# Optimization experiments

Hardware: AMD Instinct MI355X
Metric: run time of the kernel (lower is better)

## Reference

```python
import jax, jax.numpy as jnp
import numpy as np
from jax import lax

NPOINT = 1024
RADIUS = 0.2
NSAMPLE = 32
BN_EPS = 1e-5


def fps(xyz, npoint):
    """Deterministic farthest point sampling (start index 0). xyz: (B,N,3) -> (B,npoint) int32."""
    B, N, _ = xyz.shape

    def step(carry, _):
        distance, farthest = carry
        centroid = jnp.take_along_axis(xyz, farthest[:, None, None], axis=1)  # (B,1,3)
        d = jnp.sum((xyz - centroid) ** 2, axis=-1)  # (B,N)
        distance = jnp.minimum(distance, d)
        nxt = jnp.argmax(distance, axis=-1).astype(jnp.int32)
        return (distance, nxt), farthest

    init = (jnp.full((B, N), jnp.inf, dtype=xyz.dtype), jnp.zeros((B,), jnp.int32))
    _, idxs = lax.scan(step, init, None, length=npoint)  # (npoint, B)
    return jnp.transpose(idxs)  # (B, npoint)


def ball_query(radius, nsample, xyz, new_xyz):
    """Deterministic ball query: first nsample in-radius indices (sorted), padded with first hit.
    xyz: (B,N,3), new_xyz: (B,S,3) -> (B,S,nsample) int32."""
    B, N, _ = xyz.shape
    # squared distances via GEMM form to avoid (B,S,N,3) intermediate
    sqr = (jnp.sum(new_xyz ** 2, -1)[:, :, None]
           + jnp.sum(xyz ** 2, -1)[:, None, :]
           - 2.0 * jnp.einsum('bsd,bnd->bsn', new_xyz, xyz))  # (B,S,N)
    idx = jnp.where(sqr <= radius ** 2, jnp.arange(N, dtype=jnp.int32), N)
    idx = jnp.sort(idx, axis=-1)[:, :, :nsample]  # (B,S,K)
    first = idx[:, :, :1]
    first = jnp.where(first == N, 0, first)  # no point in radius -> index 0
    return jnp.where(idx == N, first, idx)


def setup_inputs() -> dict:
    key = jax.random.key(0)
    ks = jax.random.split(key, 8)
    B, N, Cin = 16, 4096, 64
    xyz = jax.random.uniform(ks[0], (B, N, 3), dtype=jnp.float32)
    points = jax.random.normal(ks[1], (B, Cin, N), dtype=jnp.float32)
    chans = [Cin + 3, 64, 64, 128]
    d = {"xyz": xyz, "points": points}
    for i in range(3):
        d[f"w{i}"] = jax.random.normal(ks[2 + i], (chans[i + 1], chans[i]), dtype=jnp.float32) / np.float32(np.sqrt(chans[i]))
        d[f"g{i}"] = jnp.ones((chans[i + 1],), dtype=jnp.float32)
        d[f"b{i}"] = jnp.zeros((chans[i + 1],), dtype=jnp.float32)
    return d


def _forward(xyz, points, params):
    B, N, _ = xyz.shape
    idx = fps(xyz, NPOINT)                                     # (B,S)
    new_xyz = jnp.take_along_axis(xyz, idx[:, :, None], axis=1)  # (B,S,3)
    gidx = ball_query(RADIUS, NSAMPLE, xyz, new_xyz)             # (B,S,K)
    gather = jax.vmap(lambda p, i: p[i])
    grouped_xyz = gather(xyz, gidx) - new_xyz[:, :, None, :]     # (B,S,K,3)
    grouped_pts = gather(jnp.transpose(points, (0, 2, 1)), gidx)  # (B,S,K,C)
    feats = jnp.concatenate([grouped_xyz, grouped_pts], axis=-1)  # (B,S,K,3+C)
    for (w, g, b) in params:
        feats = jnp.einsum('oc,bskc->bsko', w, feats)
        mean = jnp.mean(feats, axis=(0, 1, 2))
        var = jnp.var(feats, axis=(0, 1, 2))
        feats = (feats - mean) * (g * lax.rsqrt(var + BN_EPS)) + b  # BatchNorm (batch stats)
        feats = jax.nn.relu(feats)
    feats = jnp.max(feats, axis=2)               # (B,S,Cout) max-pool over neighbors
    return new_xyz, jnp.transpose(feats, (0, 2, 1))  # (B,Cout,S) channel-first like torch


def reference(xyz, points, w0, g0, b0, w1, g1, b1, w2, g2, b2):
    params = [(w0, g0, b0), (w1, g1, b1), (w2, g2, b2)]
    return _forward(xyz, points, params)
```

## Files before the change

kernel.cpp:

```cpp
#include <hip/hip_runtime.h>

#define DI static __device__ __forceinline__

typedef float v2f __attribute__((ext_vector_type(2)));
typedef __attribute__((ext_vector_type(8))) short bf16x8;
typedef __attribute__((ext_vector_type(4))) float f32x4;

DI unsigned short f2bf(float f) {
  unsigned int u = __float_as_uint(f);
  u = (u + 0x7fffu + ((u >> 16) & 1u)) >> 16;
  return (unsigned short)u;
}
DI float bf2f(unsigned short h) { return __uint_as_float(((unsigned int)h) << 16); }

#define DPP_MAXU(v, ctrl)                                                      \
  {                                                                            \
    unsigned o_ = (unsigned)__builtin_amdgcn_update_dpp((int)(v), (int)(v),    \
                                                        (ctrl), 0xf, 0xf, false); \
    (v) = (o_ > (v)) ? o_ : (v);                                               \
  }
#define DPP_MINU(v, ctrl)                                                      \
  {                                                                            \
    unsigned o_ = (unsigned)__builtin_amdgcn_update_dpp((int)(v), (int)(v),    \
                                                        (ctrl), 0xf, 0xf, false); \
    (v) = (o_ < (v)) ? o_ : (v);                                               \
  }

__global__ __launch_bounds__(256) void fps_kernel(const float* __restrict__ xyz,
                                                  float* __restrict__ newxyz) {
  const int b = blockIdx.x;
  const int t = threadIdx.x;
  const int lane = t & 63, wid = t >> 6;
  const float* X = xyz + (size_t)b * 4096 * 3;
  __shared__ float XL[4096 * 3];
  __shared__ int FI[1024];
  __shared__ unsigned long long slot[2][4];
  for (int idx = t; idx < 12288; idx += 256) XL[idx] = X[idx];
  v2f px[8], py[8], pz[8], dist[8];
#pragma unroll
  for (int q = 0; q < 8; ++q) {
    int i0 = t + (q << 9);
    int i1 = i0 + 256;
    px[q] = (v2f){X[i0 * 3 + 0], X[i1 * 3 + 0]};
    py[q] = (v2f){X[i0 * 3 + 1], X[i1 * 3 + 1]};
    pz[q] = (v2f){X[i0 * 3 + 2], X[i1 * 3 + 2]};
    dist[q] = (v2f){3.402823466e38f, 3.402823466e38f};
  }
  __syncthreads();
  float cx = XL[0], cy = XL[1], cz = XL[2];
  int fi = 0;
  for (int s = 0; s < 1024; ++s) {
    if (t == 0) FI[s] = fi;
    float bv = -1.0f;
    unsigned int bi = 0;
    v2f cxv = (v2f){cx, cx}, cyv = (v2f){cy, cy}, czv = (v2f){cz, cz};
#pragma unroll
    for (int q = 0; q < 8; ++q) {
#pragma clang fp contract(off)
      v2f dx = px[q] - cxv;
      v2f dy = py[q] - cyv;
      v2f dz = pz[q] - czv;
      v2f d = (dx * dx + dy * dy) + dz * dz;
#if __has_builtin(__builtin_elementwise_min)
      v2f nd = __builtin_elementwise_min(dist[q], d);
#else
      v2f nd;
      nd.x = fminf(dist[q].x, d.x);
      nd.y = fminf(dist[q].y, d.y);
#endif
      dist[q] = nd;
      float n0 = nd.x, n1 = nd.y;
      bool c0 = (n0 > bv);
      bv = c0 ? n0 : bv;
      bi = c0 ? (unsigned)(t + (q << 9)) : bi;
      bool c1 = (n1 > bv);
      bv = c1 ? n1 : bv;
      bi = c1 ? (unsigned)(t + (q << 9) + 256) : bi;
    }
    unsigned vb = __float_as_uint(bv);
    unsigned m = vb;
    DPP_MAXU(m, 0x111);
    DPP_MAXU(m, 0x112);
    DPP_MAXU(m, 0x114);
    DPP_MAXU(m, 0x118);
    DPP_MAXU(m, 0x142);
    DPP_MAXU(m, 0x143);
    unsigned wmax = (unsigned)__builtin_amdgcn_readlane((int)m, 63);
    unsigned ik = (vb == wmax) ? bi : 0xFFFFFFFFu;
    DPP_MINU(ik, 0x111);
    DPP_MINU(ik, 0x112);
    DPP_MINU(ik, 0x114);
    DPP_MINU(ik, 0x118);
    DPP_MINU(ik, 0x142);
    DPP_MINU(ik, 0x143);
    unsigned widx = (unsigned)__builtin_amdgcn_readlane((int)ik, 63);
    const int p = s & 1;
    if (lane == 0)
      slot[p][wid] = ((unsigned long long)wmax << 32) | (unsigned long long)(~widx);
    __syncthreads();
    unsigned long long k0 = slot[p][0], k1 = slot[p][1];
    unsigned long long k2 = slot[p][2], k3 = slot[p][3];
    unsigned long long m01 = (k0 >= k1) ? k0 : k1;
    unsigned long long m23 = (k2 >= k3) ? k2 : k3;
    unsigned long long win = (m01 >= m23) ? m01 : m23;
    fi = (int)(~(unsigned int)win);
    cx = XL[fi * 3 + 0];
    cy = XL[fi * 3 + 1];
    cz = XL[fi * 3 + 2];
  }
  __syncthreads();
  float* out = newxyz + (size_t)b * 1024 * 3;
  for (int s2 = t; s2 < 1024; s2 += 256) {
    int f = FI[s2];
    out[s2 * 3 + 0] = XL[f * 3 + 0];
    out[s2 * 3 + 1] = XL[f * 3 + 1];
    out[s2 * 3 + 2] = XL[f * 3 + 2];
  }
}

__global__ __launch_bounds__(256) void p0_kernel(const float* __restrict__ points,
                                                 const float* __restrict__ w0,
                                                 float* __restrict__ P0) {
  const int b = blockIdx.x >> 6;
  const int n0 = (blockIdx.x & 63) << 6;
  const int t = threadIdx.x;
  __shared__ float W[64][64];
  for (int idx = t; idx < 4096; idx += 256) {
    int c = idx >> 6, o = idx & 63;
    W[c][o] = w0[o * 67 + 3 + c];
  }
  __syncthreads();
  const int i = t >> 4, j = t & 15;
  const float* Pb = points + (size_t)b * 64 * 4096 + n0 + 4 * i;
  float acc[4][4] = {};
  for (int c = 0; c < 64; ++c) {
    float4 xv = *(const float4*)(Pb + (size_t)c * 4096);
    float4 wv = *(const float4*)&W[c][4 * j];
    float xr[4] = {xv.x, xv.y, xv.z, xv.w};
    float wr[4] = {wv.x, wv.y, wv.z, wv.w};
#pragma unroll
    for (int rr = 0; rr < 4; ++rr)
#pragma unroll
      for (int oi = 0; oi < 4; ++oi) acc[rr][oi] = fmaf(xr[rr], wr[oi], acc[rr][oi]);
  }
#pragma unroll
  for (int rr = 0; rr < 4; ++rr) {
    float4 vv = make_float4(acc[rr][0], acc[rr][1], acc[rr][2], acc[rr][3]);
    *(float4*)(P0 + ((size_t)b * 4096 + n0 + 4 * i + rr) * 64 + 4 * j) = vv;
  }
}

__global__ __launch_bounds__(256) void ballquery_stats0_kernel(
    const float* __restrict__ xyz, const float* __restrict__ newxyz,
    const float* __restrict__ P0, const float* __restrict__ w0,
    int* __restrict__ gidx, float* __restrict__ partials0) {
  const int t = threadIdx.x;
  const int lane = t & 63, w = t >> 6;
  const int gid = blockIdx.x * 4 + w;
  const int b = gid >> 10;
  __shared__ int sel[4][32];
  __shared__ float red[4][128];
  const float* Xb = xyz + (size_t)b * 4096 * 3;
  const float cx = newxyz[(size_t)gid * 3 + 0];
  const float cy = newxyz[(size_t)gid * 3 + 1];
  const float cz = newxyz[(size_t)gid * 3 + 2];
  const float cs = __fadd_rn(__fadd_rn(__fmul_rn(cx, cx), __fmul_rn(cy, cy)), __fmul_rn(cz, cz));
  int cnt = 0, first = 0;
  bool found = false;
  for (int base = 0; base < 4096; base += 64) {
    int i = base + lane;
    float x = Xb[i * 3 + 0], y = Xb[i * 3 + 1], z = Xb[i * 3 + 2];
    float xs = __fadd_rn(__fadd_rn(__fmul_rn(x, x), __fmul_rn(y, y)), __fmul_rn(z, z));
    float dot = fmaf(cz, z, fmaf(cy, y, __fmul_rn(cx, x)));
    float sqr = __fsub_rn(__fadd_rn(cs, xs), __fmul_rn(2.0f, dot));
    bool ok = sqr <= 0.04f;
    unsigned long long mask = __ballot(ok);
    if (!found && mask != 0ull) { first = base + __builtin_ctzll(mask); found = true; }
    int pre = __popcll(mask & ((1ull << lane) - 1ull));
    int pos = cnt + pre;
    if (ok && pos < 32) sel[w][pos] = i;
    cnt += (int)__popcll(mask);
    if (cnt >= 32) break;
  }
  if (cnt < 32) {
    int pad = found ? first : 0;
    for (int p = cnt + lane; p < 32; p += 64) sel[w][p] = pad;
  }
  __syncthreads();
  if (lane < 32) gidx[(size_t)gid * 32 + lane] = sel[w][lane];
  const int c = lane;
  float wx = w0[c * 67 + 0], wy = w0[c * 67 + 1], wz = w0[c * 67 + 2];
  float ssum = 0.f, ssq = 0.f;
  const float* P0b = P0 + (size_t)b * 4096 * 64;
  for (int k = 0; k < 32; ++k) {
    int g = sel[w][k];
    float gx = Xb[g * 3 + 0] - cx, gy = Xb[g * 3 + 1] - cy, gz = Xb[g * 3 + 2] - cz;
    float a0 = fmaf(wx, gx, fmaf(wy, gy, fmaf(wz, gz, P0b[(size_t)g * 64 + c])));
    ssum += a0;
    ssq = fmaf(a0, a0, ssq);
  }
  red[w][c] = ssum;
  red[w][c + 64] = ssq;
  __syncthreads();
  if (t < 128) {
    float acc = red[0][t] + red[1][t] + red[2][t] + red[3][t];
    partials0[(size_t)t * 4096 + blockIdx.x] = acc;
  }
}

__global__ __launch_bounds__(256) void finalize_kernel(
    const float* __restrict__ partials, int C, int nblk,
    const float* __restrict__ gamma, const float* __restrict__ beta,
    float* __restrict__ scale, float* __restrict__ shift) {
  const int c = blockIdx.x, t = threadIdx.x;
  double s1 = 0.0, s2 = 0.0;
  for (int k = t; k < nblk; k += 256) {
    s1 += (double)partials[(size_t)c * nblk + k];
    s2 += (double)partials[(size_t)(C + c) * nblk + k];
  }
  __shared__ double r1[256], r2[256];
  r1[t] = s1;
  r2[t] = s2;
  __syncthreads();
  for (int off = 128; off > 0; off >>= 1) {
    if (t < off) { r1[t] += r1[t + off]; r2[t] += r2[t + off]; }
    __syncthreads();
  }
  if (t == 0) {
    const double M = 524288.0;
    double mean = r1[0] / M;
    double var = r2[0] / M - mean * mean;
    if (var < 0.0) var = 0.0;
    float sc = gamma[c] * (float)(1.0 / sqrt(var + 1e-5));
    scale[c] = sc;
    shift[c] = beta[c] - (float)mean * sc;
  }
}

__global__ __launch_bounds__(256) void p2_kernel(
    const float* __restrict__ xyz, const float* __restrict__ newxyz,
    const float* __restrict__ P0, const int* __restrict__ gidx,
    const float* __restrict__ w0, const float* __restrict__ w1,
    const float* __restrict__ sc0g, const float* __restrict__ sh0g,
    unsigned short* __restrict__ act1, float* __restrict__ partials1) {
  __shared__ float W1s[64][64];
  __shared__ float Xs[64][64];
  __shared__ float w0x[64], w0y[64], w0z[64], sc0[64], sh0[64];
  __shared__ float Sred[256][8];
  const int t = threadIdx.x;
  for (int idx = t; idx < 4096; idx += 256) {
    int c = idx >> 6, o = idx & 63;
    W1s[c][o] = w1[o * 64 + c];
  }
  if (t < 64) {
    w0x[t] = w0[t * 67 + 0];
    w0y[t] = w0[t * 67 + 1];
    w0z[t] = w0[t * 67 + 2];
    sc0[t] = sc0g[t];
    sh0[t] = sh0g[t];
  }
  __syncthreads();
  const int i = t >> 4, j = t & 15;
  const int rl = t >> 2, cq = t & 3;
  float ssum[4] = {}, ssq[4] = {};
  for (int tile = 0; tile < 8; ++tile) {
    const int rowbase = (blockIdx.x * 8 + tile) << 6;
    {
      int r = rowbase + rl;
      int b = r >> 15, s = (r >> 5) & 1023;
      int g = gidx[r];
      const float* Pt = xyz + ((size_t)b * 4096 + g) * 3;
      const float* Ct = newxyz + ((size_t)b * 1024 + s) * 3;
      float dx = Pt[0] - Ct[0], dy = Pt[1] - Ct[1], dz = Pt[2] - Ct[2];
      const float* p0r = P0 + ((size_t)b * 4096 + g) * 64 + cq * 16;
      const float4* p4 = (const float4*)p0r;
      float4 a0 = p4[0], a1 = p4[1], a2 = p4[2], a3 = p4[3];
      float pv[16] = {a0.x, a0.y, a0.z, a0.w, a1.x, a1.y, a1.z, a1.w,
                      a2.x, a2.y, a2.z, a2.w, a3.x, a3.y, a3.z, a3.w};
#pragma unroll
      for (int cc = 0; cc < 16; ++cc) {
        int c = cq * 16 + cc;
        float a = fmaf(w0x[c], dx, fmaf(w0y[c], dy, fmaf(w0z[c], dz, pv[cc])));
        Xs[c][rl] = fmaxf(0.f, fmaf(a, sc0[c], sh0[c]));
      }
    }
    __syncthreads();
    float acc[4][4] = {};
#pragma unroll 4
    for (int c = 0; c < 64; ++c) {
      float4 xv = *(const float4*)&Xs[c][4 * i];
      float4 wv = *(const float4*)&W1s[c][4 * j];
      float xr[4] = {xv.x, xv.y, xv.z, xv.w};
      float wr[4] = {wv.x, wv.y, wv.z, wv.w};
#pragma unroll
      for (int rr = 0; rr < 4; ++rr)
#pragma unroll
        for (int oi = 0; oi < 4; ++oi) acc[rr][oi] = fmaf(xr[rr], wr[oi], acc[rr][oi]);
    }
#pragma unroll
    for (int rr = 0; rr < 4; ++rr) {
      size_t r = (size_t)rowbase + 4 * i + rr;
      ushort4 pk;
      float y0 = acc[rr][0], y1 = acc[rr][1], y2 = acc[rr][2], y3 = acc[rr][3];
      ssum[0] += y0; ssq[0] = fmaf(y0, y0, ssq[0]);
      ssum[1] += y1; ssq[1] = fmaf(y1, y1, ssq[1]);
      ssum[2] += y2; ssq[2] = fmaf(y2, y2, ssq[2]);
      ssum[3] += y3; ssq[3] = fmaf(y3, y3, ssq[3]);
      pk.x = f2bf(y0); pk.y = f2bf(y1); pk.z = f2bf(y2); pk.w = f2bf(y3);
      *(ushort4*)(act1 + r * 64 + 4 * j) = pk;
    }
    __syncthreads();
  }
#pragma unroll
  for (int oi = 0; oi < 4; ++oi) { Sred[t][oi] = ssum[oi]; Sred[t][4 + oi] = ssq[oi]; }
  __syncthreads();
  if (t < 64) {
    int jj = t >> 2, oi = t & 3;
    float s1 = 0.f, s2 = 0.f;
#pragma unroll
    for (int ii = 0; ii < 16; ++ii) {
      s1 += Sred[ii * 16 + jj][oi];
      s2 += Sred[ii * 16 + jj][4 + oi];
    }
    partials1[(size_t)t * 1024 + blockIdx.x] = s1;
    partials1[(size_t)(64 + t) * 1024 + blockIdx.x] = s2;
  }
}

__global__ __launch_bounds__(256) void p3_kernel(
    const unsigned short* __restrict__ act1, const float* __restrict__ w2,
    const float* __restrict__ sc1g, const float* __restrict__ sh1g,
    float* __restrict__ partials2, float* __restrict__ gmx,
    float* __restrict__ gmn) {
  __shared__ unsigned short W2T[128 * 72];
  __shared__ unsigned short A[64 * 72];
  __shared__ float Mred[4][132], Nred[4][132];
  __shared__ float S1r[4][132], S2r[4][132];
  __shared__ float sc1[64], sh1[64];
  const int t = threadIdx.x;
  const int lane = t & 63, w = t >> 6;
  const int quad = lane >> 4, l15 = lane & 15;
  for (int idx = t; idx < 8192; idx += 256) {
    int o = idx >> 6, c = idx & 63;
    W2T[o * 72 + c] = f2bf(w2[o * 64 + c]);
  }
  if (t < 64) { sc1[t] = sc1g[t]; sh1[t] = sh1g[t]; }
  __syncthreads();
  const int rl = t >> 2, cq = t & 3;
  float ssum[8] = {}, ssq[8] = {};
  for (int tile = 0; tile < 8; ++tile) {
    const int rowbase = (blockIdx.x * 8 + tile) << 6;
    {
      size_t r = (size_t)rowbase + rl;
      const uint4* pr = (const uint4*)(act1 + r * 64 + cq * 16);
      uint4 aa = pr[0], bb = pr[1];
      unsigned int uu[8] = {aa.x, aa.y, aa.z, aa.w, bb.x, bb.y, bb.z, bb.w};
      unsigned int pk[8];
#pragma unroll
      for (int q = 0; q < 8; ++q) {
        int c = cq * 16 + 2 * q;
        float v0 = bf2f((unsigned short)(uu[q] & 0xffffu));
        float v1 = bf2f((unsigned short)(uu[q] >> 16));
        float r0 = fmaxf(0.f, fmaf(v0, sc1[c], sh1[c]));
        float r1 = fmaxf(0.f, fmaf(v1, sc1[c + 1], sh1[c + 1]));
        pk[q] = (unsigned)f2bf(r0) | ((unsigned)f2bf(r1) << 16);
      }
      uint4* dst = (uint4*)&A[rl * 72 + cq * 16];
      dst[0] = make_uint4(pk[0], pk[1], pk[2], pk[3]);
      dst[1] = make_uint4(pk[4], pk[5], pk[6], pk[7]);
    }
    __syncthreads();
    const unsigned short* Arow = &A[(w * 16 + l15) * 72 + quad * 8];
    bf16x8 a0 = *(const bf16x8*)(Arow);
    bf16x8 a1 = *(const bf16x8*)(Arow + 32);
    f32x4 acc[8];
#pragma unroll
    for (int nt = 0; nt < 8; ++nt) {
      const unsigned short* Brow = &W2T[(nt * 16 + l15) * 72 + quad * 8];
      bf16x8 b0 = *(const bf16x8*)(Brow);
      bf16x8 b1 = *(const bf16x8*)(Brow + 32);
      f32x4 c0 = {0.f, 0.f, 0.f, 0.f};
      c0 = __builtin_amdgcn_mfma_f32_16x16x32_bf16(a0, b0, c0, 0, 0, 0);
      c0 = __builtin_amdgcn_mfma_f32_16x16x32_bf16(a1, b1, c0, 0, 0, 0);
      acc[nt] = c0;
    }
#pragma unroll
    for (int nt = 0; nt < 8; ++nt) {
      float y0 = acc[nt][0], y1 = acc[nt][1], y2 = acc[nt][2], y3 = acc[nt][3];
      ssum[nt] += ((y0 + y1) + (y2 + y3));
      ssq[nt] = fmaf(y0, y0, ssq[nt]);
      ssq[nt] = fmaf(y1, y1, ssq[nt]);
      ssq[nt] = fmaf(y2, y2, ssq[nt]);
      ssq[nt] = fmaf(y3, y3, ssq[nt]);
      float mx = fmaxf(fmaxf(y0, y1), fmaxf(y2, y3));
      float mn = fminf(fminf(y0, y1), fminf(y2, y3));
      mx = fmaxf(mx, __shfl_xor(mx, 16, 64));
      mx = fmaxf(mx, __shfl_xor(mx, 32, 64));
      mn = fminf(mn, __shfl_xor(mn, 16, 64));
      mn = fminf(mn, __shfl_xor(mn, 32, 64));
      if (quad == 0) {
        Mred[w][nt * 16 + l15] = mx;
        Nred[w][nt * 16 + l15] = mn;
      }
    }
    __syncthreads();
    {
      int o = t & 127, g = t >> 7;
      float mx = fmaxf(Mred[2 * g][o], Mred[2 * g + 1][o]);
      float mn = fminf(Nred[2 * g][o], Nred[2 * g + 1][o]);
      int bb2 = rowbase >> 15;
      int ss2 = ((rowbase >> 5) & 1023) + g;
      size_t oidx = ((size_t)bb2 * 128 + o) * 1024 + ss2;
      gmx[oidx] = mx;
      gmn[oidx] = mn;
    }
    __syncthreads();
  }
#pragma unroll
  for (int nt = 0; nt < 8; ++nt) {
    float s1 = ssum[nt];
    s1 += __shfl_xor(s1, 16, 64);
    s1 += __shfl_xor(s1, 32, 64);
    float s2 = ssq[nt];
    s2 += __shfl_xor(s2, 16, 64);
    s2 += __shfl_xor(s2, 32, 64);
    if (quad == 0) {
      S1r[w][nt * 16 + l15] = s1;
      S2r[w][nt * 16 + l15] = s2;
    }
  }
  __syncthreads();
  if (t < 128) {
    int o = t;
    float s1 = S1r[0][o] + S1r[1][o] + S1r[2][o] + S1r[3][o];
    float s2 = S2r[0][o] + S2r[1][o] + S2r[2][o] + S2r[3][o];
    partials2[(size_t)o * 1024 + blockIdx.x] = s1;
    partials2[(size_t)(128 + o) * 1024 + blockIdx.x] = s2;
  }
}

__global__ __launch_bounds__(256) void p4f_kernel(
    const float* __restrict__ gmx, const float* __restrict__ gmn,
    const float* __restrict__ sc2g, const float* __restrict__ sh2g,
    float* __restrict__ feats) {
  const int bo = blockIdx.x >> 2;
  const int s = ((blockIdx.x & 3) << 8) + threadIdx.x;
  const int o = bo & 127;
  const float sc = sc2g[o], sh = sh2g[o];
  size_t idx = (size_t)bo * 1024 + s;
  float v = (sc >= 0.f) ? gmx[idx] : gmn[idx];
  feats[idx] = fmaxf(0.f, fmaf(v, sc, sh));
}

extern "C" void kernel_launch(void* const* d_in, const int* in_sizes, int n_in,
                              void* d_out, int out_size, void* d_ws, size_t ws_size,
                              hipStream_t stream) {
  const float* xyz = (const float*)d_in[0];
  const float* points = (const float*)d_in[1];
  const float* w0 = (const float*)d_in[2];
  const float* g0 = (const float*)d_in[3];
  const float* b0 = (const float*)d_in[4];
  const float* w1 = (const float*)d_in[5];
  const float* g1 = (const float*)d_in[6];
  const float* b1 = (const float*)d_in[7];
  const float* w2 = (const float*)d_in[8];
  const float* g2 = (const float*)d_in[9];
  const float* b2 = (const float*)d_in[10];

  float* out = (float*)d_out;
  float* newxyz = out;
  float* feats = out + 49152;

  char* ws = (char*)d_ws;
  float* P0 = (float*)ws;
  float* gmx = (float*)ws;
  float* gmn = (float*)(ws + (size_t)(8u << 20));
  int* gidx = (int*)(ws + (size_t)(16u << 20));
  unsigned short* act1 = (unsigned short*)(ws + (size_t)(18u << 20));
  float* partials0 = (float*)(ws + (size_t)(82u << 20));
  float* partials1 = (float*)(ws + (size_t)(84u << 20));
  float* partials2 = (float*)(ws + (size_t)(85u << 20));
  float* sc0 = (float*)(ws + (size_t)(86u << 20));
  float* sh0 = sc0 + 128;
  float* sc1 = sc0 + 256;
  float* sh1 = sc0 + 384;
  float* sc2 = sc0 + 512;
  float* sh2 = sc0 + 640;

  fps_kernel<<<16, 256, 0, stream>>>(xyz, newxyz);
  p0_kernel<<<1024, 256, 0, stream>>>(points, w0, P0);
  ballquery_stats0_kernel<<<4096, 256, 0, stream>>>(xyz, newxyz, P0, w0, gidx, partials0);
  finalize_kernel<<<64, 256, 0, stream>>>(partials0, 64, 4096, g0, b0, sc0, sh0);
  p2_kernel<<<1024, 256, 0, stream>>>(xyz, newxyz, P0, gidx, w0, w1, sc0, sh0, act1, partials1);
  finalize_kernel<<<64, 256, 0, stream>>>(partials1, 64, 1024, g1, b1, sc1, sh1);
  p3_kernel<<<1024, 256, 0, stream>>>(act1, w2, sc1, sh1, partials2, gmx, gmn);
  finalize_kernel<<<128, 256, 0, stream>>>(partials2, 128, 1024, g2, b2, sc2, sh2);
  p4f_kernel<<<8192, 256, 0, stream>>>(gmx, gmn, sc2, sh2, feats);
}
```

Before: 922.0 us.

## Use bf16 MFMA for layer-1 GEMM and packed f32 ops in FPS

The second-layer 64x64 GEMM in p2_kernel moves from scalar FP32 FMA over shared-memory tiles to bf16 MFMA 16x16x32, with inputs and weights converted to bf16 in padded LDS. The BN statistics reduction now uses wave shuffles instead of a large shared array. Separately, the FPS distance computation is forced onto v_pk_add/v_pk_mul inline asm. The MFMA path lowers precision of the layer-1 input, and the act1 stores become scattered 2-byte writes, which may reduce store efficiency.

Measured after the change: 938.8 us. About the same (+1.8%).

```diff
diff --git a/kernel.cpp b/kernel.cpp
--- a/kernel.cpp
+++ b/kernel.cpp
@@ -12,6 +12,22 @@
   return (unsigned short)u;
 }
 DI float bf2f(unsigned short h) { return __uint_as_float(((unsigned int)h) << 16); }
+
+DI v2f pk_sub(v2f a, v2f b) {
+  v2f d;
+  asm("v_pk_add_f32 %0, %1, %2 neg_lo:[0,1] neg_hi:[0,1]" : "=v"(d) : "v"(a), "v"(b));
+  return d;
+}
+DI v2f pk_mul(v2f a, v2f b) {
+  v2f d;
+  asm("v_pk_mul_f32 %0, %1, %2" : "=v"(d) : "v"(a), "v"(b));
+  return d;
+}
+DI v2f pk_add(v2f a, v2f b) {
+  v2f d;
+  asm("v_pk_add_f32 %0, %1, %2" : "=v"(d) : "v"(a), "v"(b));
+  return d;
+}
 
 #define DPP_MAXU(v, ctrl)                                                      \
   {                                                                            \
@@ -56,20 +72,14 @@
     v2f cxv = (v2f){cx, cx}, cyv = (v2f){cy, cy}, czv = (v2f){cz, cz};
 #pragma unroll
     for (int q = 0; q < 8; ++q) {
-#pragma clang fp contract(off)
-      v2f dx = px[q] - cxv;
-      v2f dy = py[q] - cyv;
-      v2f dz = pz[q] - czv;
-      v2f d = (dx * dx + dy * dy) + dz * dz;
-#if __has_builtin(__builtin_elementwise_min)
-      v2f nd = __builtin_elementwise_min(dist[q], d);
-#else
-      v2f nd;
-      nd.x = fminf(dist[q].x, d.x);
-      nd.y = fminf(dist[q].y, d.y);
-#endif
-      dist[q] = nd;
-      float n0 = nd.x, n1 = nd.y;
+      v2f dx = pk_sub(px[q], cxv);
+      v2f dy = pk_sub(py[q], cyv);
+      v2f dz = pk_sub(pz[q], czv);
+      v2f d = pk_add(pk_add(pk_mul(dx, dx), pk_mul(dy, dy)), pk_mul(dz, dz));
+      float n0 = fminf(dist[q].x, d.x);
+      float n1 = fminf(dist[q].y, d.y);
+      dist[q].x = n0;
+      dist[q].y = n1;
       bool c0 = (n0 > bv);
       bv = c0 ? n0 : bv;
       bi = c0 ? (unsigned)(t + (q << 9)) : bi;
@@ -243,14 +253,16 @@
     const float* __restrict__ w0, const float* __restrict__ w1,
     const float* __restrict__ sc0g, const float* __restrict__ sh0g,
     unsigned short* __restrict__ act1, float* __restrict__ partials1) {
-  __shared__ float W1s[64][64];
-  __shared__ float Xs[64][64];
+  __shared__ unsigned short W1T[64 * 72];
+  __shared__ unsigned short A[64 * 72];
+  __shared__ float S1r[4][68], S2r[4][68];
   __shared__ float w0x[64], w0y[64], w0z[64], sc0[64], sh0[64];
-  __shared__ float Sred[256][8];
   const int t = threadIdx.x;
+  const int lane = t & 63, w = t >> 6;
+  const int quad = lane >> 4, l15 = lane & 15;
   for (int idx = t; idx < 4096; idx += 256) {
-    int c = idx >> 6, o = idx & 63;
-    W1s[c][o] = w1[o * 64 + c];
+    int o = idx >> 6, c = idx & 63;
+    W1T[o * 72 + c] = f2bf(w1[o * 64 + c]);
   }
   if (t < 64) {
     w0x[t] = w0[t * 67 + 0];
@@ -260,7 +272,6 @@
     sh0[t] = sh0g[t];
   }
   __syncthreads();
-  const int i = t >> 4, j = t & 15;
   const int rl = t >> 2, cq = t & 3;
   float ssum[4] = {}, ssq[4] = {};
   for (int tile = 0; tile < 8; ++tile) {
@@ -272,58 +283,68 @@
       const float* Pt = xyz + ((size_t)b * 4096 + g) * 3;
       const float* Ct = newxyz + ((size_t)b * 1024 + s) * 3;
       float dx = Pt[0] - Ct[0], dy = Pt[1] - Ct[1], dz = Pt[2] - Ct[2];
-      const float* p0r = P0 + ((size_t)b * 4096 + g) * 64 + cq * 16;
-      const float4* p4 = (const float4*)p0r;
+      const float4* p4 = (const float4*)(P0 + ((size_t)b * 4096 + g) * 64 + cq * 16);
       float4 a0 = p4[0], a1 = p4[1], a2 = p4[2], a3 = p4[3];
       float pv[16] = {a0.x, a0.y, a0.z, a0.w, a1.x, a1.y, a1.z, a1.w,
                       a2.x, a2.y, a2.z, a2.w, a3.x, a3.y, a3.z, a3.w};
-#pragma unroll
-      for (int cc = 0; cc < 16; ++cc) {
-        int c = cq * 16 + cc;
-        float a = fmaf(w0x[c], dx, fmaf(w0y[c], dy, fmaf(w0z[c], dz, pv[cc])));
-        Xs[c][rl] = fmaxf(0.f, fmaf(a, sc0[c], sh0[c]));
+      unsigned pk[8];
+#pragma unroll
+      for (int q = 0; q < 8; ++q) {
+        int c0 = cq * 16 + 2 * q, c1 = c0 + 1;
+        float aa = fmaf(w0x[c0], dx, fmaf(w0y[c0], dy, fmaf(w0z[c0], dz, pv[2 * q])));
+        float bb = fmaf(w0x[c1], dx, fmaf(w0y[c1], dy, fmaf(w0z[c1], dz, pv[2 * q + 1])));
+        float r0 = fmaxf(0.f, fmaf(aa, sc0[c0], sh0[c0]));
+        float r1 = fmaxf(0.f, fmaf(bb, sc0[c1], sh0[c1]));
+        pk[q] = (unsigned)f2bf(r0) | ((unsigned)f2bf(r1) << 16);
       }
-    }
-    __syncthreads();
-    float acc[4][4] = {};
-#pragma unroll 4
-    for (int c = 0; c < 64; ++c) {
-      float4 xv = *(const float4*)&Xs[c][4 * i];
-      float4 wv = *(const float4*)&W1s[c][4 * j];
-      float xr[4] = {xv.x, xv.y, xv.z, xv.w};
-      float wr[4] = {wv.x, wv.y, wv.z, wv.w};
-#pragma unroll
-      for (int rr = 0; rr < 4; ++rr)
-#pragma unroll
-        for (int oi = 0; oi < 4; ++oi) acc[rr][oi] = fmaf(xr[rr], wr[oi], acc[rr][oi]);
-    }
-#pragma unroll
-    for (int rr = 0; rr < 4; ++rr) {
-      size_t r = (size_t)rowbase + 4 * i + rr;
-      ushort4 pk;
-      float y0 = acc[rr][0], y1 = acc[rr][1], y2 = acc[rr][2], y3 = acc[rr][3];
-      ssum[0] += y0; ssq[0] = fmaf(y0, y0, ssq[0]);
-      ssum[1] += y1; ssq[1] = fmaf(y1, y1, ssq[1]);
-      ssum[2] += y2; ssq[2] = fmaf(y2, y2, ssq[2]);
-      ssum[3] += y3; ssq[3] = fmaf(y3, y3, ssq[3]);
-      pk.x = f2bf(y0); pk.y = f2bf(y1); pk.z = f2bf(y2); pk.w = f2bf(y3);
-      *(ushort4*)(act1 + r * 64 + 4 * j) = pk;
-    }
-    __syncthreads();
-  }
-#pragma unroll
-  for (int oi = 0; oi < 4; ++oi) { Sred[t][oi] = ssum[oi]; Sred[t][4 + oi] = ssq[oi]; }
+      uint4* dst = (uint4*)&A[rl * 72 + cq * 16];
+      dst[0] = make_uint4(pk[0], pk[1], pk[2], pk[3]);
+      dst[1] = make_uint4(pk[4], pk[5], pk[6], pk[7]);
+    }
+    __syncthreads();
+    const unsigned short* Arow = &A[(w * 16 + l15) * 72 + quad * 8];
+    bf16x8 a0 = *(const bf16x8*)(Arow);
+    bf16x8 a1 = *(const bf16x8*)(Arow + 32);
+#pragma unroll
+    for (int nt = 0; nt < 4; ++nt) {
+      const unsigned short* Brow = &W1T[(nt * 16 + l15) * 72 + quad * 8];
+      bf16x8 b0 = *(const bf16x8*)(Brow);
+      bf16x8 b1 = *(const bf16x8*)(Brow + 32);
+      f32x4 c0 = {0.f, 0.f, 0.f, 0.f};
+      c0 = __builtin_amdgcn_mfma_f32_16x16x32_bf16(a0, b0, c0, 0, 0, 0);
+      c0 = __builtin_amdgcn_mfma_f32_16x16x32_bf16(a1, b1, c0, 0, 0, 0);
+      size_t rbase = (size_t)rowbase + w * 16 + quad * 4;
+      int o = nt * 16 + l15;
+#pragma unroll
+      for (int reg = 0; reg < 4; ++reg) {
+        float y = c0[reg];
+        ssum[nt] += y;
+        ssq[nt] = fmaf(y, y, ssq[nt]);
+        act1[(rbase + reg) * 64 + o] = f2bf(y);
+      }
+    }
+    __syncthreads();
+  }
+#pragma unroll
+  for (int nt = 0; nt < 4; ++nt) {
+    float s1 = ssum[nt];
+    s1 += __shfl_xor(s1, 16, 64);
+    s1 += __shfl_xor(s1, 32, 64);
+    float s2 = ssq[nt];
+    s2 += __shfl_xor(s2, 16, 64);
+    s2 += __shfl_xor(s2, 32, 64);
+    if (quad == 0) {
+      S1r[w][nt * 16 + l15] = s1;
+      S2r[w][nt * 16 + l15] = s2;
+    }
+  }
   __syncthreads();
   if (t < 64) {
-    int jj = t >> 2, oi = t & 3;
-    float s1 = 0.f, s2 = 0.f;
-#pragma unroll
-    for (int ii = 0; ii < 16; ++ii) {
-      s1 += Sred[ii * 16 + jj][oi];
-      s2 += Sred[ii * 16 + jj][4 + oi];
-    }
-    partials1[(size_t)t * 1024 + blockIdx.x] = s1;
-    partials1[(size_t)(64 + t) * 1024 + blockIdx.x] = s2;
+    int o = t;
+    float s1 = S1r[0][o] + S1r[1][o] + S1r[2][o] + S1r[3][o];
+    float s2 = S2r[0][o] + S2r[1][o] + S2r[2][o] + S2r[3][o];
+    partials1[(size_t)o * 1024 + blockIdx.x] = s1;
+    partials1[(size_t)(64 + o) * 1024 + blockIdx.x] = s2;
   }
 }
 
```
